# Kernel optimization log

Hardware: AMD Instinct MI355X
Metric: run time of the kernel (lower is better)

The kernel has to match this reference:

```python
import jax, jax.numpy as jnp
import numpy as np

N = 50000
E = 800000
NUM_GRAPHS = 64
D_IN = 261
D_SAGE = 64
D_LIN = 32
N_SAGE_REST = 6
N_LIN_REST = 3
EPS = 1e-5


def _layernorm(x, g, b):
    mu = jnp.mean(x, axis=-1, keepdims=True)
    var = jnp.mean((x - mu) ** 2, axis=-1, keepdims=True)
    return (x - mu) * jax.lax.rsqrt(var + EPS) * g + b


def _sage_block(x, Wl, bl, Wr, g, b, src, dst, inv_deg, residual):
    # mean aggregation of neighbor (source) features onto targets
    msum = jax.ops.segment_sum(x[src], dst, num_segments=N)  # [N, d]
    mean = msum * inv_deg  # [N, d]
    f = mean @ Wl + bl + x @ Wr  # lin_l(aggr) + lin_r(x); lin_r has no bias
    f = jax.nn.gelu(f, approximate=False)
    f = _layernorm(f, g, b)
    if residual:
        f = f + x
    return f


def _lin_block(x, W, b, g, beta, residual):
    f = jax.nn.gelu(x @ W + b, approximate=False)
    f = _layernorm(f, g, beta)
    if residual:
        f = f + x
    return f


def setup_inputs() -> dict:
    key = jax.random.key(0)
    ks = jax.random.split(key, 24)
    x = jax.random.normal(ks[0], (N, D_IN), dtype=jnp.float32)
    edge_index = jax.random.randint(ks[1], (2, E), 0, N, dtype=jnp.int64)
    batch = jnp.sort(jax.random.randint(ks[2], (N,), 0, NUM_GRAPHS, dtype=jnp.int64))

    def glorot(k, shape):
        fan_in = shape[0]
        return jax.random.normal(k, shape, dtype=jnp.float32) / np.sqrt(fan_in)

    inp = {
        "x": x, "edge_index": edge_index, "batch": batch,
        # first SAGE block (261 -> 64, no residual)
        "Wl0": glorot(ks[3], (D_IN, D_SAGE)), "bl0": jnp.zeros((D_SAGE,), jnp.float32),
        "Wr0": glorot(ks[4], (D_IN, D_SAGE)),
        "g0": jnp.ones((D_SAGE,), jnp.float32), "beta0": jnp.zeros((D_SAGE,), jnp.float32),
        # 6 residual SAGE blocks (64 -> 64), stacked
        "Wl": glorot(ks[5], (N_SAGE_REST, D_SAGE, D_SAGE)),
        "bl": jnp.zeros((N_SAGE_REST, D_SAGE), jnp.float32),
        "Wr": glorot(ks[6], (N_SAGE_REST, D_SAGE, D_SAGE)),
        "g": jnp.ones((N_SAGE_REST, D_SAGE), jnp.float32),
        "beta": jnp.zeros((N_SAGE_REST, D_SAGE), jnp.float32),
        # MLP: first LinearBlock 64 -> 32 (no residual)
        "M0": glorot(ks[7], (D_SAGE, D_LIN)), "mb0": jnp.zeros((D_LIN,), jnp.float32),
        "mg0": jnp.ones((D_LIN,), jnp.float32), "mbeta0": jnp.zeros((D_LIN,), jnp.float32),
        # 3 residual LinearBlocks 32 -> 32, stacked
        "M": glorot(ks[8], (N_LIN_REST, D_LIN, D_LIN)),
        "mb": jnp.zeros((N_LIN_REST, D_LIN), jnp.float32),
        "mg": jnp.ones((N_LIN_REST, D_LIN), jnp.float32),
        "mbeta": jnp.zeros((N_LIN_REST, D_LIN), jnp.float32),
        # final Linear 32 -> 1
        "Wf": glorot(ks[9], (D_LIN, 1)), "bf": jnp.zeros((1,), jnp.float32),
    }
    return inp


def reference(x, edge_index, batch, Wl0, bl0, Wr0, g0, beta0, Wl, bl, Wr, g, beta,
              M0, mb0, mg0, mbeta0, M, mb, mg, mbeta, Wf, bf):
    src, dst = edge_index[0], edge_index[1]
    deg = jax.ops.segment_sum(jnp.ones((E,), x.dtype), dst, num_segments=N)
    inv_deg = (1.0 / jnp.maximum(deg, 1.0))[:, None]  # [N,1]

    h = _sage_block(x, Wl0, bl0, Wr0, g0, beta0, src, dst, inv_deg, residual=False)
    for i in range(N_SAGE_REST):
        h = _sage_block(h, Wl[i], bl[i], Wr[i], g[i], beta[i], src, dst, inv_deg, residual=True)

    pooled = jax.ops.segment_sum(h, batch, num_segments=NUM_GRAPHS)  # [G, 64]

    m = _lin_block(pooled, M0, mb0, mg0, mbeta0, residual=False)
    for i in range(N_LIN_REST):
        m = _lin_block(m, M[i], mb[i], mg[i], mbeta[i], residual=True)
    return m @ Wf + bf  # [G, 1]
```

## Files before the change

kernel.cpp:

```cpp
#include <hip/hip_runtime.h>
#include <hip/hip_bf16.h>
#include <math.h>

#define N_NODES 50000
#define N_EDGES 800000
#define NUM_GRAPHS 64
#define NPAD 50048
#define KPAD0 288
#define PSPLIT 16
#define MAXDEG 64

#define GEMM0_GRID (NPAD / 64)
#define SCAT_GRID  ((N_EDGES + 255) / 256)
#define ZERO_GRID  ((N_NODES + 255) / 256)
#define PREPW_TOT  (128 * KPAD0 + 6 * 128 * 64)
#define PREPW_GRID ((PREPW_TOT + 255) / 256)

typedef __attribute__((ext_vector_type(8))) short short8;
typedef __attribute__((ext_vector_type(4))) float f32x4;

__device__ __forceinline__ float gelu_f(float v) {
    return 0.5f * v * (1.0f + erff(v * 0.70710678118654752440f));
}

__device__ __forceinline__ float half_sum32(float v) {
    v += __shfl_xor(v, 1); v += __shfl_xor(v, 2); v += __shfl_xor(v, 4);
    v += __shfl_xor(v, 8); v += __shfl_xor(v, 16);
    return v;
}

__device__ __forceinline__ float group_sum8(float v) {
    v += __shfl_xor(v, 1); v += __shfl_xor(v, 2); v += __shfl_xor(v, 4);
    return v;
}

__device__ __forceinline__ unsigned short f2bf(float f) {
    unsigned int u = __float_as_uint(f);
    unsigned int r = (u + 0x7fffu + ((u >> 16) & 1u)) >> 16;
    return (unsigned short)r;
}

__device__ __forceinline__ float bf_lo(unsigned int u) {
    return __uint_as_float(u << 16);
}
__device__ __forceinline__ float bf_hi(unsigned int u) {
    return __uint_as_float(u & 0xffff0000u);
}


__global__ void k_prep(int* __restrict__ deg,
                       const float* __restrict__ Wl0, const float* __restrict__ Wr0,
                       const float* __restrict__ Wl, const float* __restrict__ Wr,
                       unsigned short* __restrict__ Bt0, unsigned short* __restrict__ BtR) {
    const int blk = blockIdx.x, tid = threadIdx.x;
    if (blk < ZERO_GRID) {
        int i = blk * 256 + tid;
        if (i < N_NODES) deg[i] = 0;
        return;
    }
    int idx = (blk - ZERO_GRID) * 256 + tid;
    const int n0 = 128 * KPAD0;
    if (idx < n0) {
        int j = idx / KPAD0, k = idx - j * KPAD0;
        float v = 0.0f;
        if (k < 261) v = (j < 64) ? Wl0[k * 64 + j] : Wr0[k * 64 + (j - 64)];
        Bt0[idx] = f2bf(v);
    } else if (idx < PREPW_TOT) {
        int r = idx - n0;
        int l = r >> 13;
        int rr = r & 8191;
        int j = rr >> 6, k = rr & 63;
        float v = (j < 64) ? Wl[l * 4096 + k * 64 + j] : Wr[l * 4096 + k * 64 + (j - 64)];
        BtR[r] = f2bf(v);
    }
}


__global__ __launch_bounds__(256) void k_front(
        const float* __restrict__ X, const unsigned short* __restrict__ Bt0,
        unsigned short* __restrict__ U, float* __restrict__ V,
        const int* __restrict__ src, const int* __restrict__ dst,
        int* __restrict__ deg, unsigned short* __restrict__ col64) {
    __shared__ __align__(16) unsigned short sA[64 * 32];
    __shared__ __align__(16) unsigned short sB[128 * 32];
    const int blk = blockIdx.x;
    const int tid = threadIdx.x;

    if (blk < GEMM0_GRID) {
        const int lane = tid & 63, wid = tid >> 6;
        const int l16 = lane & 15, quad = lane >> 4;
        const int m0 = blk * 64;
        f32x4 acc[8];
        #pragma unroll
        for (int j = 0; j < 8; ++j) { acc[j][0] = 0.f; acc[j][1] = 0.f; acc[j][2] = 0.f; acc[j][3] = 0.f; }
        const int arow = tid >> 2, apart = (tid & 3) << 3;
        const int node = m0 + arow;
        const int rowok = (node < N_NODES);
        for (int kc = 0; kc < KPAD0; kc += 32) {
            if (kc) __syncthreads();
            short8 av;
            #pragma unroll
            for (int j = 0; j < 8; ++j) {
                int kk = kc + apart + j;
                float val = (rowok && kk < 261) ? X[(size_t)node * 261 + kk] : 0.0f;
                av[j] = (short)f2bf(val);
            }
            *(short8*)&sA[arow * 32 + apart] = av;
            #pragma unroll
            for (int q = 0; q < 2; ++q) {
                int flat = q * 256 + tid;
                int br = flat >> 2, bp = (flat & 3) << 3;
                *(int4*)&sB[br * 32 + bp] = *(const int4*)&Bt0[(size_t)br * KPAD0 + kc + bp];
            }
            __syncthreads();
            short8 af = *(const short8*)&sA[(wid * 16 + l16) * 32 + quad * 8];
            #pragma unroll
            for (int j = 0; j < 8; ++j) {
                short8 bf = *(const short8*)&sB[(j * 16 + l16) * 32 + quad * 8];
                acc[j] = __builtin_amdgcn_mfma_f32_16x16x32_bf16(af, bf, acc[j], 0, 0, 0);
            }
        }
        const int rbase = m0 + wid * 16 + quad * 4;
        #pragma unroll
        for (int j = 0; j < 4; ++j)
            #pragma unroll
            for (int r = 0; r < 4; ++r)
                U[(size_t)(rbase + r) * 64 + j * 16 + l16] = f2bf(acc[j][r]);
        #pragma unroll
        for (int j = 4; j < 8; ++j)
            #pragma unroll
            for (int r = 0; r < 4; ++r)
                V[(size_t)(rbase + r) * 64 + (j - 4) * 16 + l16] = acc[j][r];
    } else {
        int i = (blk - GEMM0_GRID) * 256 + tid;
        if (i < N_EDGES) {
            int d = dst[i];
            int pos = atomicAdd(&deg[d], 1);
            if (pos < MAXDEG) col64[(d << 6) + pos] = (unsigned short)src[i];
        }
    }
}


__global__ __launch_bounds__(256) void k_layer(
        const unsigned short* __restrict__ U_in, const float* __restrict__ V_in,
        unsigned short* __restrict__ h,
        float* __restrict__ hf_out,
        const int* __restrict__ deg, const unsigned short* __restrict__ col64,
        const float* __restrict__ bias, const float* __restrict__ gam,
        const float* __restrict__ bet,
        const unsigned short* __restrict__ Bt_next,
        unsigned short* __restrict__ U_out, float* __restrict__ V_out,
        int residual, int have_gemm) {
    __shared__ __align__(16) unsigned short sA[2 * 64 * 32];
    __shared__ __align__(16) unsigned short sB[128 * 32];
    const int tid = threadIdx.x;
    const int lane = tid & 63, wid = tid >> 6;
    const int sub = lane >> 3, hl = lane & 7;
    const int base = lane & 56;
    const int m0 = blockIdx.x * 64;
    const uint4* __restrict__ Up = (const uint4*)U_in;

    #pragma unroll
    for (int rep = 0; rep < 2; ++rep) {
        const int nl = rep * 32 + wid * 8 + sub;
        const int node = m0 + nl;
        const bool valid = (node < N_NODES);
        const int nd = valid ? node : 0;
        const int dg = valid ? deg[nd] : 0;
        const int cnt = min(dg, MAXDEG);
        uint4 cv = make_uint4(0u, 0u, 0u, 0u);
        if (valid) cv = *(const uint4*)&col64[((size_t)nd << 6) + hl * 8];
        float s0 = 0.f, s1 = 0.f, s2 = 0.f, s3 = 0.f, s4 = 0.f, s5 = 0.f, s6 = 0.f, s7 = 0.f;
        for (int b = 0; b * 8 < cnt; b += 2) {
            #pragma unroll
            for (int hh = 0; hh < 2; ++hh) {
                const int sl = base + b + hh;
                unsigned int p0 = (unsigned int)__shfl((int)cv.x, sl);
                unsigned int p1 = (unsigned int)__shfl((int)cv.y, sl);
                unsigned int p2 = (unsigned int)__shfl((int)cv.z, sl);
                unsigned int p3 = (unsigned int)__shfl((int)cv.w, sl);
                const int eb = (b + hh) * 8;
                int c[8];
                c[0] = (int)(p0 & 0xffffu); c[1] = (int)(p0 >> 16);
                c[2] = (int)(p1 & 0xffffu); c[3] = (int)(p1 >> 16);
                c[4] = (int)(p2 & 0xffffu); c[5] = (int)(p2 >> 16);
                c[6] = (int)(p3 & 0xffffu); c[7] = (int)(p3 >> 16);
                #pragma unroll
                for (int i = 0; i < 8; ++i) {
                    uint4 u = (eb + i < cnt) ? Up[(size_t)c[i] * 8 + hl] : make_uint4(0u, 0u, 0u, 0u);
                    s0 += bf_lo(u.x); s1 += bf_hi(u.x);
                    s2 += bf_lo(u.y); s3 += bf_hi(u.y);
                    s4 += bf_lo(u.z); s5 += bf_hi(u.z);
                    s6 += bf_lo(u.w); s7 += bf_hi(u.w);
                }
            }
        }
        const float id = 1.0f / fmaxf((float)dg, 1.0f);
        const float4 b0 = *(const float4*)&bias[8 * hl];
        const float4 b1 = *(const float4*)&bias[8 * hl + 4];
        float4 v0 = make_float4(0.f, 0.f, 0.f, 0.f), v1 = v0;
        if (valid) {
            v0 = *(const float4*)&V_in[(size_t)nd * 64 + 8 * hl];
            v1 = *(const float4*)&V_in[(size_t)nd * 64 + 8 * hl + 4];
        }
        float f0 = gelu_f(s0 * id + b0.x + v0.x);
        float f1 = gelu_f(s1 * id + b0.y + v0.y);
        float f2 = gelu_f(s2 * id + b0.z + v0.z);
        float f3 = gelu_f(s3 * id + b0.w + v0.w);
        float f4 = gelu_f(s4 * id + b1.x + v1.x);
        float f5 = gelu_f(s5 * id + b1.y + v1.y);
        float f6 = gelu_f(s6 * id + b1.z + v1.z);
        float f7 = gelu_f(s7 * id + b1.w + v1.w);
        float mu = group_sum8(((f0 + f1) + (f2 + f3)) + ((f4 + f5) + (f6 + f7))) * 0.015625f;
        float d0 = f0 - mu, d1 = f1 - mu, d2 = f2 - mu, d3 = f3 - mu;
        float d4 = f4 - mu, d5 = f5 - mu, d6 = f6 - mu, d7 = f7 - mu;
        float var = group_sum8(((d0 * d0 + d1 * d1) + (d2 * d2 + d3 * d3)) +
                               ((d4 * d4 + d5 * d5) + (d6 * d6 + d7 * d7))) * 0.015625f;
        float rs = rsqrtf(var + 1e-5f);
        const float4 g0v = *(const float4*)&gam[8 * hl];
        const float4 g1v = *(const float4*)&gam[8 * hl + 4];
        const float4 e0v = *(const float4*)&bet[8 * hl];
        const float4 e1v = *(const float4*)&bet[8 * hl + 4];
        f0 = d0 * rs * g0v.x + e0v.x;
        f1 = d1 * rs * g0v.y + e0v.y;
        f2 = d2 * rs * g0v.z + e0v.z;
        f3 = d3 * rs * g0v.w + e0v.w;
        f4 = d4 * rs * g1v.x + e1v.x;
        f5 = d5 * rs * g1v.y + e1v.y;
        f6 = d6 * rs * g1v.z + e1v.z;
        f7 = d7 * rs * g1v.w + e1v.w;
        if (residual && valid) {
            uint4 hu = ((const uint4*)h)[(size_t)nd * 8 + hl];
            f0 += bf_lo(hu.x); f1 += bf_hi(hu.x);
            f2 += bf_lo(hu.y); f3 += bf_hi(hu.y);
            f4 += bf_lo(hu.z); f5 += bf_hi(hu.z);
            f6 += bf_lo(hu.w); f7 += bf_hi(hu.w);
        }
        uint4 outw;
        outw.x = (unsigned int)f2bf(f0) | ((unsigned int)f2bf(f1) << 16);
        outw.y = (unsigned int)f2bf(f2) | ((unsigned int)f2bf(f3) << 16);
        outw.z = (unsigned int)f2bf(f4) | ((unsigned int)f2bf(f5) << 16);
        outw.w = (unsigned int)f2bf(f6) | ((unsigned int)f2bf(f7) << 16);
        if (valid) {
            ((uint4*)h)[(size_t)nd * 8 + hl] = outw;
            if (hf_out) {
                *(float4*)&hf_out[(size_t)nd * 64 + 8 * hl] = make_float4(f0, f1, f2, f3);
                *(float4*)&hf_out[(size_t)nd * 64 + 8 * hl + 4] = make_float4(f4, f5, f6, f7);
            }
        }
        *(uint4*)&sA[(((hl >> 2) * 64 + nl) << 5) + (hl & 3) * 8] = outw;
    }
    if (!have_gemm) return;
    __syncthreads();

    const int l16 = lane & 15, quad = lane >> 4;
    f32x4 acc[8];
    #pragma unroll
    for (int j = 0; j < 8; ++j) { acc[j][0] = 0.f; acc[j][1] = 0.f; acc[j][2] = 0.f; acc[j][3] = 0.f; }
    for (int kc = 0; kc < 64; kc += 32) {
        if (kc) __syncthreads();
        #pragma unroll
        for (int q = 0; q < 2; ++q) {
            int flat = q * 256 + tid;
            int br = flat >> 2, bp = (flat & 3) << 3;
            *(int4*)&sB[br * 32 + bp] = *(const int4*)&Bt_next[(size_t)br * 64 + kc + bp];
        }
        __syncthreads();
        short8 af = *(const short8*)&sA[(((kc >> 5) * 64 + wid * 16 + l16) << 5) + quad * 8];
        #pragma unroll
        for (int j = 0; j < 8; ++j) {
            short8 bf = *(const short8*)&sB[(j * 16 + l16) * 32 + quad * 8];
            acc[j] = __builtin_amdgcn_mfma_f32_16x16x32_bf16(af, bf, acc[j], 0, 0, 0);
        }
    }
    const int rbase = m0 + wid * 16 + quad * 4;
    #pragma unroll
    for (int j = 0; j < 4; ++j)
        #pragma unroll
        for (int r = 0; r < 4; ++r)
            U_out[(size_t)(rbase + r) * 64 + j * 16 + l16] = f2bf(acc[j][r]);
    #pragma unroll
    for (int j = 4; j < 8; ++j)
        #pragma unroll
        for (int r = 0; r < 4; ++r)
            V_out[(size_t)(rbase + r) * 64 + (j - 4) * 16 + l16] = acc[j][r];
}


__global__ __launch_bounds__(256) void k_pool1(const float* __restrict__ h, const int* __restrict__ batch,
                                               float* __restrict__ partial, int n) {
    __shared__ float sred[4][64];
    const int g = blockIdx.x / PSPLIT;
    const int s = blockIdx.x - g * PSPLIT;
    const int lane = threadIdx.x & 63, wid = threadIdx.x >> 6;
    int lo = 0, hi = n;
    while (lo < hi) { int mid = (lo + hi) >> 1; if (batch[mid] < g) lo = mid + 1; else hi = mid; }
    const int start = lo;
    lo = 0; hi = n;
    while (lo < hi) { int mid = (lo + hi) >> 1; if (batch[mid] < g + 1) lo = mid + 1; else hi = mid; }
    const int end = lo;
    const int len = end - start;
    const int chunk = (len + PSPLIT - 1) / PSPLIT;
    const int a = start + s * chunk;
    const int b = min(a + chunk, end);
    float sum = 0.0f;
    for (int node = a + wid; node < b; node += 4) sum += h[(size_t)node * 64 + lane];
    sred[wid][lane] = sum;
    __syncthreads();
    if (wid == 0)
        partial[(size_t)blockIdx.x * 64 + lane] = sred[0][lane] + sred[1][lane] + sred[2][lane] + sred[3][lane];
}


__global__ __launch_bounds__(1024) void k_head(const float* __restrict__ partial,
                                               const float* __restrict__ M0, const float* __restrict__ mb0,
                                               const float* __restrict__ mg0, const float* __restrict__ mbeta0,
                                               const float* __restrict__ M, const float* __restrict__ mb,
                                               const float* __restrict__ mg, const float* __restrict__ mbeta,
                                               const float* __restrict__ Wf, const float* __restrict__ bf,
                                               float* __restrict__ out) {
    __shared__ float sP[64 * 64];
    __shared__ float sA[64 * 33];
    __shared__ float sB[64 * 33];
    const int tx = threadIdx.x, ty = threadIdx.y;
    const int tid = ty * 32 + tx;
    for (int i = tid; i < 64 * 64; i += 1024) {
        int g = i >> 6, f = i & 63;
        float s = 0.0f;
        #pragma unroll
        for (int s2 = 0; s2 < PSPLIT; ++s2) s += partial[(size_t)(g * PSPLIT + s2) * 64 + f];
        sP[i] = s;
    }
    __syncthreads();
    #pragma unroll
    for (int rr = 0; rr < 2; ++rr) {
        int r = ty + rr * 32;
        float a = mb0[tx];
        for (int k = 0; k < 64; ++k) a += sP[r * 64 + k] * M0[k * 32 + tx];
        a = gelu_f(a);
        float mu = half_sum32(a) * (1.0f / 32.0f);
        float d = a - mu;
        float var = half_sum32(d * d) * (1.0f / 32.0f);
        a = d * rsqrtf(var + 1e-5f) * mg0[tx] + mbeta0[tx];
        sA[r * 33 + tx] = a;
    }
    __syncthreads();
    float* cur = sA;
    float* nxt = sB;
    for (int L = 0; L < 3; ++L) {
        const float* Mi = M + L * 32 * 32;
        const float* mbi = mb + L * 32;
        const float* mgi = mg + L * 32;
        const float* mbetai = mbeta + L * 32;
        #pragma unroll
        for (int rr = 0; rr < 2; ++rr) {
            int r = ty + rr * 32;
            float a = mbi[tx];
            for (int k = 0; k < 32; ++k) a += cur[r * 33 + k] * Mi[k * 32 + tx];
            a = gelu_f(a);
            float mu = half_sum32(a) * (1.0f / 32.0f);
            float d = a - mu;
            float var = half_sum32(d * d) * (1.0f / 32.0f);
            a = d * rsqrtf(var + 1e-5f) * mgi[tx] + mbetai[tx] + cur[r * 33 + tx];
            nxt[r * 33 + tx] = a;
        }
        __syncthreads();
        float* t = cur; cur = nxt; nxt = t;
    }
    #pragma unroll
    for (int rr = 0; rr < 2; ++rr) {
        int r = ty + rr * 32;
        float p = cur[r * 33 + tx] * Wf[tx];
        p = half_sum32(p);
        if (tx == 0) out[r] = p + bf[0];
    }
}


extern "C" void kernel_launch(void* const* d_in, const int* in_sizes, int n_in,
                              void* d_out, int out_size, void* d_ws, size_t ws_size,
                              hipStream_t stream) {
    const int N = N_NODES;
    const int E = N_EDGES;

    const float* x    = (const float*)d_in[0];
    const int* eidx   = (const int*)d_in[1];
    const int* batch  = (const int*)d_in[2];
    const float* Wl0  = (const float*)d_in[3];
    const float* bl0  = (const float*)d_in[4];
    const float* Wr0  = (const float*)d_in[5];
    const float* g0   = (const float*)d_in[6];
    const float* bet0 = (const float*)d_in[7];
    const float* Wl   = (const float*)d_in[8];
    const float* bl   = (const float*)d_in[9];
    const float* Wr   = (const float*)d_in[10];
    const float* gR   = (const float*)d_in[11];
    const float* betR = (const float*)d_in[12];
    const float* M0   = (const float*)d_in[13];
    const float* mb0  = (const float*)d_in[14];
    const float* mg0  = (const float*)d_in[15];
    const float* mbe0 = (const float*)d_in[16];
    const float* M    = (const float*)d_in[17];
    const float* mb   = (const float*)d_in[18];
    const float* mg   = (const float*)d_in[19];
    const float* mbe  = (const float*)d_in[20];
    const float* Wf   = (const float*)d_in[21];
    const float* bf   = (const float*)d_in[22];

    const int* src = eidx;
    const int* dst = eidx + E;

    char* p = (char*)d_ws;
    auto alloc = [&](size_t bytes) -> void* {
        void* q = (void*)p;
        p += (bytes + 255) & ~(size_t)255;
        return q;
    };
    int*   deg    = (int*)alloc((size_t)N * 4);
    unsigned short* col64 = (unsigned short*)alloc((size_t)N * MAXDEG * 2);
    unsigned short* Bt0 = (unsigned short*)alloc((size_t)128 * KPAD0 * 2);
    unsigned short* BtR = (unsigned short*)alloc((size_t)6 * 128 * 64 * 2);
    unsigned short* Ua  = (unsigned short*)alloc((size_t)NPAD * 64 * 2);
    unsigned short* Ub  = (unsigned short*)alloc((size_t)NPAD * 64 * 2);
    float* Va   = (float*)alloc((size_t)NPAD * 64 * 4);
    float* Vb   = (float*)alloc((size_t)NPAD * 64 * 4);
    unsigned short* hbuf = (unsigned short*)alloc((size_t)NPAD * 64 * 2);
    float* partial = (float*)alloc((size_t)NUM_GRAPHS * PSPLIT * 64 * 4);

    k_prep<<<ZERO_GRID + PREPW_GRID, 256, 0, stream>>>(deg, Wl0, Wr0, Wl, Wr, Bt0, BtR);

    k_front<<<GEMM0_GRID + SCAT_GRID, 256, 0, stream>>>(
        x, Bt0, Ua, Va, src, dst, deg, col64);

    unsigned short* Uin = Ua;  float* Vin = Va;
    unsigned short* Uout = Ub; float* Vout = Vb;
    for (int i = 0; i < 7; ++i) {
        const float* bias = (i == 0) ? bl0  : bl  + (size_t)(i - 1) * 64;
        const float* gam  = (i == 0) ? g0   : gR  + (size_t)(i - 1) * 64;
        const float* bet  = (i == 0) ? bet0 : betR + (size_t)(i - 1) * 64;
        const int have_gemm = (i < 6);
        float* hf = (i == 6) ? Vout : nullptr;
        k_layer<<<GEMM0_GRID, 256, 0, stream>>>(
            Uin, Vin, hbuf, hf, deg, col64, bias, gam, bet,
            have_gemm ? (BtR + (size_t)i * 128 * 64) : BtR,
            Uout, Vout, (i > 0) ? 1 : 0, have_gemm);
        unsigned short* tu = Uin; Uin = Uout; Uout = tu;
        float* tv = Vin; Vin = Vout; Vout = tv;
    }
    float* hf_final = Vin;

    k_pool1<<<NUM_GRAPHS * PSPLIT, 256, 0, stream>>>(hf_final, batch, partial, N);
    k_head<<<1, dim3(32, 32), 0, stream>>>(partial, M0, mb0, mg0, mbe0, M, mb, mg, mbe, Wf, bf, (float*)d_out);
}
```

Baseline: 405.9 us.

## Fuse graph sum-pooling into last SAGE layer via shared-memory atomics

The final SAGE layer now accumulates per-graph sums directly. It uses shared-memory atomics keyed by graph id, falling back to global atomics when a block's 64 nodes span more than 8 graphs, and flushes the block's partial sums to a global pooled buffer. This removes the fp32 hidden-state write, the separate pooling kernel with its binary searches, and the partial-sum reduction in the head. The scatter of the adjacency list also switches to nontemporal stores. The cost is float atomic contention and non-deterministic summation order.

```diff
diff --git a/kernel.cpp b/kernel.cpp
--- a/kernel.cpp
+++ b/kernel.cpp
@@ -7,7 +7,6 @@
 #define NUM_GRAPHS 64
 #define NPAD 50048
 #define KPAD0 288
-#define PSPLIT 16
 #define MAXDEG 64
 
 #define GEMM0_GRID (NPAD / 64)
@@ -48,7 +47,7 @@
 }
 
 
-__global__ void k_prep(int* __restrict__ deg,
+__global__ void k_prep(int* __restrict__ deg, float* __restrict__ pooled,
                        const float* __restrict__ Wl0, const float* __restrict__ Wr0,
                        const float* __restrict__ Wl, const float* __restrict__ Wr,
                        unsigned short* __restrict__ Bt0, unsigned short* __restrict__ BtR) {
@@ -56,6 +55,7 @@
     if (blk < ZERO_GRID) {
         int i = blk * 256 + tid;
         if (i < N_NODES) deg[i] = 0;
+        if (i < NUM_GRAPHS * 64) pooled[i] = 0.0f;
         return;
     }
     int idx = (blk - ZERO_GRID) * 256 + tid;
@@ -136,7 +136,8 @@
         if (i < N_EDGES) {
             int d = dst[i];
             int pos = atomicAdd(&deg[d], 1);
-            if (pos < MAXDEG) col64[(d << 6) + pos] = (unsigned short)src[i];
+            if (pos < MAXDEG)
+                __builtin_nontemporal_store((unsigned short)src[i], &col64[(d << 6) + pos]);
         }
     }
 }
@@ -145,21 +146,32 @@
 __global__ __launch_bounds__(256) void k_layer(
         const unsigned short* __restrict__ U_in, const float* __restrict__ V_in,
         unsigned short* __restrict__ h,
-        float* __restrict__ hf_out,
         const int* __restrict__ deg, const unsigned short* __restrict__ col64,
         const float* __restrict__ bias, const float* __restrict__ gam,
         const float* __restrict__ bet,
         const unsigned short* __restrict__ Bt_next,
         unsigned short* __restrict__ U_out, float* __restrict__ V_out,
+        const int* __restrict__ batch, float* __restrict__ pooled,
         int residual, int have_gemm) {
     __shared__ __align__(16) unsigned short sA[2 * 64 * 32];
     __shared__ __align__(16) unsigned short sB[128 * 32];
+    __shared__ float sPool[8 * 64];
     const int tid = threadIdx.x;
     const int lane = tid & 63, wid = tid >> 6;
     const int sub = lane >> 3, hl = lane & 7;
     const int base = lane & 56;
     const int m0 = blockIdx.x * 64;
     const uint4* __restrict__ Up = (const uint4*)U_in;
+    const int is_last = (pooled != nullptr);
+
+    int gmin = 0, span = 1;
+    if (is_last) {
+        gmin = batch[m0];
+        int gmax = batch[min(m0 + 63, N_NODES - 1)];
+        span = gmax - gmin + 1;
+        for (int i = tid; i < 8 * 64; i += 256) sPool[i] = 0.0f;
+        __syncthreads();
+    }
 
     #pragma unroll
     for (int rep = 0; rep < 2; ++rep) {
@@ -237,19 +249,44 @@
             f4 += bf_lo(hu.z); f5 += bf_hi(hu.z);
             f6 += bf_lo(hu.w); f7 += bf_hi(hu.w);
         }
-        uint4 outw;
-        outw.x = (unsigned int)f2bf(f0) | ((unsigned int)f2bf(f1) << 16);
-        outw.y = (unsigned int)f2bf(f2) | ((unsigned int)f2bf(f3) << 16);
-        outw.z = (unsigned int)f2bf(f4) | ((unsigned int)f2bf(f5) << 16);
-        outw.w = (unsigned int)f2bf(f6) | ((unsigned int)f2bf(f7) << 16);
         if (valid) {
-            ((uint4*)h)[(size_t)nd * 8 + hl] = outw;
-            if (hf_out) {
-                *(float4*)&hf_out[(size_t)nd * 64 + 8 * hl] = make_float4(f0, f1, f2, f3);
-                *(float4*)&hf_out[(size_t)nd * 64 + 8 * hl + 4] = make_float4(f4, f5, f6, f7);
+            if (!is_last) {
+                uint4 outw;
+                outw.x = (unsigned int)f2bf(f0) | ((unsigned int)f2bf(f1) << 16);
+                outw.y = (unsigned int)f2bf(f2) | ((unsigned int)f2bf(f3) << 16);
+                outw.z = (unsigned int)f2bf(f4) | ((unsigned int)f2bf(f5) << 16);
+                outw.w = (unsigned int)f2bf(f6) | ((unsigned int)f2bf(f7) << 16);
+                ((uint4*)h)[(size_t)nd * 8 + hl] = outw;
+                *(uint4*)&sA[(((hl >> 2) * 64 + nl) << 5) + (hl & 3) * 8] = outw;
+            } else {
+                int g = batch[nd];
+                if (span <= 8) {
+                    float* pp = &sPool[(g - gmin) * 64 + 8 * hl];
+                    atomicAdd(&pp[0], f0); atomicAdd(&pp[1], f1);
+                    atomicAdd(&pp[2], f2); atomicAdd(&pp[3], f3);
+                    atomicAdd(&pp[4], f4); atomicAdd(&pp[5], f5);
+                    atomicAdd(&pp[6], f6); atomicAdd(&pp[7], f7);
+                } else {
+                    float* pp = &pooled[(size_t)g * 64 + 8 * hl];
+                    atomicAdd(&pp[0], f0); atomicAdd(&pp[1], f1);
+                    atomicAdd(&pp[2], f2); atomicAdd(&pp[3], f3);
+                    atomicAdd(&pp[4], f4); atomicAdd(&pp[5], f5);
+                    atomicAdd(&pp[6], f6); atomicAdd(&pp[7], f7);
+                }
             }
-        }
-        *(uint4*)&sA[(((hl >> 2) * 64 + nl) << 5) + (hl & 3) * 8] = outw;
+        } else if (!is_last) {
+            uint4 z = make_uint4(0u, 0u, 0u, 0u);
+            *(uint4*)&sA[(((hl >> 2) * 64 + nl) << 5) + (hl & 3) * 8] = z;
+        }
+    }
+
+    if (is_last) {
+        __syncthreads();
+        if (span <= 8) {
+            for (int i = tid; i < span * 64; i += 256)
+                atomicAdd(&pooled[(size_t)(gmin + (i >> 6)) * 64 + (i & 63)], sPool[i]);
+        }
+        return;
     }
     if (!have_gemm) return;
     __syncthreads();
@@ -288,32 +325,7 @@
 }
 
 
-__global__ __launch_bounds__(256) void k_pool1(const float* __restrict__ h, const int* __restrict__ batch,
-                                               float* __restrict__ partial, int n) {
-    __shared__ float sred[4][64];
-    const int g = blockIdx.x / PSPLIT;
-    const int s = blockIdx.x - g * PSPLIT;
-    const int lane = threadIdx.x & 63, wid = threadIdx.x >> 6;
-    int lo = 0, hi = n;
-    while (lo < hi) { int mid = (lo + hi) >> 1; if (batch[mid] < g) lo = mid + 1; else hi = mid; }
-    const int start = lo;
-    lo = 0; hi = n;
-    while (lo < hi) { int mid = (lo + hi) >> 1; if (batch[mid] < g + 1) lo = mid + 1; else hi = mid; }
-    const int end = lo;
-    const int len = end - start;
-    const int chunk = (len + PSPLIT - 1) / PSPLIT;
-    const int a = start + s * chunk;
-    const int b = min(a + chunk, end);
-    float sum = 0.0f;
-    for (int node = a + wid; node < b; node += 4) sum += h[(size_t)node * 64 + lane];
-    sred[wid][lane] = sum;
-    __syncthreads();
-    if (wid == 0)
-        partial[(size_t)blockIdx.x * 64 + lane] = sred[0][lane] + sred[1][lane] + sred[2][lane] + sred[3][lane];
-}
-
-
-__global__ __launch_bounds__(1024) void k_head(const float* __restrict__ partial,
+__global__ __launch_bounds__(1024) void k_head(const float* __restrict__ pooled,
                                                const float* __restrict__ M0, const float* __restrict__ mb0,
                                                const float* __restrict__ mg0, const float* __restrict__ mbeta0,
                                                const float* __restrict__ M, const float* __restrict__ mb,
@@ -325,13 +337,7 @@
     __shared__ float sB[64 * 33];
     const int tx = threadIdx.x, ty = threadIdx.y;
     const int tid = ty * 32 + tx;
-    for (int i = tid; i < 64 * 64; i += 1024) {
-        int g = i >> 6, f = i & 63;
-        float s = 0.0f;
-        #pragma unroll
-        for (int s2 = 0; s2 < PSPLIT; ++s2) s += partial[(size_t)(g * PSPLIT + s2) * 64 + f];
-        sP[i] = s;
-    }
+    for (int i = tid; i < 64 * 64; i += 1024) sP[i] = pooled[i];
     __syncthreads();
     #pragma unroll
     for (int rr = 0; rr < 2; ++rr) {
@@ -381,7 +387,6 @@
 extern "C" void kernel_launch(void* const* d_in, const int* in_sizes, int n_in,
                               void* d_out, int out_size, void* d_ws, size_t ws_size,
                               hipStream_t stream) {
-    const int N = N_NODES;
     const int E = N_EDGES;
 
     const float* x    = (const float*)d_in[0];
@@ -417,8 +422,8 @@
         p += (bytes + 255) & ~(size_t)255;
         return q;
     };
-    int*   deg    = (int*)alloc((size_t)N * 4);
-    unsigned short* col64 = (unsigned short*)alloc((size_t)N * MAXDEG * 2);
+    int*   deg    = (int*)alloc((size_t)N_NODES * 4);
+    unsigned short* col64 = (unsigned short*)alloc((size_t)N_NODES * MAXDEG * 2);
     unsigned short* Bt0 = (unsigned short*)alloc((size_t)128 * KPAD0 * 2);
     unsigned short* BtR = (unsigned short*)alloc((size_t)6 * 128 * 64 * 2);
     unsigned short* Ua  = (unsigned short*)alloc((size_t)NPAD * 64 * 2);
@@ -426,9 +431,9 @@
     float* Va   = (float*)alloc((size_t)NPAD * 64 * 4);
     float* Vb   = (float*)alloc((size_t)NPAD * 64 * 4);
     unsigned short* hbuf = (unsigned short*)alloc((size_t)NPAD * 64 * 2);
-    float* partial = (float*)alloc((size_t)NUM_GRAPHS * PSPLIT * 64 * 4);
-
-    k_prep<<<ZERO_GRID + PREPW_GRID, 256, 0, stream>>>(deg, Wl0, Wr0, Wl, Wr, Bt0, BtR);
+    float* pooled = (float*)alloc((size_t)NUM_GRAPHS * 64 * 4);
+
+    k_prep<<<ZERO_GRID + PREPW_GRID, 256, 0, stream>>>(deg, pooled, Wl0, Wr0, Wl, Wr, Bt0, BtR);
 
     k_front<<<GEMM0_GRID + SCAT_GRID, 256, 0, stream>>>(
         x, Bt0, Ua, Va, src, dst, deg, col64);
@@ -440,16 +445,14 @@
         const float* gam  = (i == 0) ? g0   : gR  + (size_t)(i - 1) * 64;
         const float* bet  = (i == 0) ? bet0 : betR + (size_t)(i - 1) * 64;
         const int have_gemm = (i < 6);
-        float* hf = (i == 6) ? Vout : nullptr;
+        float* pool_arg = (i == 6) ? pooled : nullptr;
         k_layer<<<GEMM0_GRID, 256, 0, stream>>>(
-            Uin, Vin, hbuf, hf, deg, col64, bias, gam, bet,
+            Uin, Vin, hbuf, deg, col64, bias, gam, bet,
             have_gemm ? (BtR + (size_t)i * 128 * 64) : BtR,
-            Uout, Vout, (i > 0) ? 1 : 0, have_gemm);
+            Uout, Vout, batch, pool_arg, (i > 0) ? 1 : 0, have_gemm);
         unsigned short* tu = Uin; Uin = Uout; Uout = tu;
         float* tv = Vin; Vin = Vout; Vout = tv;
     }
-    float* hf_final = Vin;
-
-    k_pool1<<<NUM_GRAPHS * PSPLIT, 256, 0, stream>>>(hf_final, batch, partial, N);
-    k_head<<<1, dim3(32, 32), 0, stream>>>(partial, M0, mb0, mg0, mbe0, M, mb, mg, mbe, Wf, bf, (float*)d_out);
-}
+
+    k_head<<<1, dim3(32, 32), 0, stream>>>(pooled, M0, mb0, mg0, mbe0, M, mb, mg, mbe, Wf, bf, (float*)d_out);
+}
```

Result: no change. 413.8 us (+1.9%).
